# Kernel tuning notes

Hardware: AMD Instinct MI355X
Metric: run time of the kernel (lower is better)

## Reference

```python
import jax, jax.numpy as jnp
import numpy as np

B, M, N = 4, 1024, 4096
DQ, DC, H, DH = 512, 512, 8, 64
D = H * DH
NEG = -10000000.0


def setup_inputs() -> dict:
    key = jax.random.key(0)
    ks = jax.random.split(key, 7)
    left = jax.random.normal(ks[0], (B, M, DQ), dtype=jnp.float32)
    right = jax.random.normal(ks[1], (B, N, DC), dtype=jnp.float32)
    mask = jax.random.randint(ks[2], (B, M, N), 0, 2).astype(bool)
    # learned params (torch Linear stores weight as (out,in); we store (in,out))
    Wq = jax.random.normal(ks[3], (DQ, D), dtype=jnp.float32) * (DQ ** -0.5)
    Wkv = jax.random.normal(ks[4], (DC, 2 * D), dtype=jnp.float32) * (DC ** -0.5)
    Wout = jax.random.normal(ks[5], (D, DQ), dtype=jnp.float32) * (D ** -0.5)
    bout = jax.random.normal(ks[6], (DQ,), dtype=jnp.float32) * 0.01
    return {"left": left, "right": right, "mask": mask,
            "Wq": Wq, "Wkv": Wkv, "Wout": Wout, "bout": bout}


def reference(left, right, mask, Wq, Wkv, Wout, bout):
    scale = DH ** -0.5
    q = left @ Wq                      # (B, M, D)
    kv = right @ Wkv                   # (B, N, 2D)
    k, v = jnp.split(kv, 2, axis=-1)   # (B, N, D) each
    q = q.reshape(B, M, H, DH).transpose(0, 2, 1, 3)  # (B, H, M, DH)
    k = k.reshape(B, N, H, DH).transpose(0, 2, 1, 3)  # (B, H, N, DH)
    v = v.reshape(B, N, H, DH).transpose(0, 2, 1, 3)  # (B, H, N, DH)
    sim = scale * jnp.einsum('bhmd,bhnd->bhmn', q, k)  # (B, H, M, N)
    sim = jnp.where(mask[:, None, :, :], sim, NEG)
    attn = jax.nn.softmax(sim, axis=-1)
    out = jnp.einsum('bhmn,bhnd->bhmd', attn, v)       # (B, H, M, DH)
    out = out.transpose(0, 2, 1, 3).reshape(B, M, D)
    return out @ Wout + bout           # (B, M, DQ)
```

## Files before the change

kernel.cpp:

```cpp
#include <hip/hip_runtime.h>

typedef _Float16 f16;
typedef __attribute__((ext_vector_type(8))) _Float16 half8;
typedef __attribute__((ext_vector_type(4))) _Float16 half4;
typedef __attribute__((ext_vector_type(4))) float floatx4;
typedef unsigned int uint32;
typedef __attribute__((ext_vector_type(4))) uint32 uint4v;

#define MFMA16(a, b, c) __builtin_amdgcn_mfma_f32_16x16x32_f16((a), (b), (c), 0, 0, 0)

constexpr int B_ = 4, M_ = 1024, N_ = 4096, DQ_ = 512, DC_ = 512, H_ = 8, DH_ = 64, D_ = 512;
constexpr int KP_ = 576;
constexpr int VP_ = 4224;
constexpr int NSPLIT = 4;
constexpr float QSC_ = 0.18033688011112042f;

typedef __attribute__((address_space(1))) const void glds_g;
typedef __attribute__((address_space(3))) void glds_l;
__device__ __forceinline__ void g2lds16(const void* g, void* l) {
    __builtin_amdgcn_global_load_lds((glds_g*)g, (glds_l*)l, 16, 0, 0);
}

__device__ __forceinline__ void wtr_tile(const float* __restrict__ src, f16* __restrict__ dst,
                                         int Nout, int bx, int by, int tid) {
    __shared__ __align__(16) f16 Ts[64][72];
    const int n0 = bx * 64, k0 = by * 64;
    {
        int kr = tid >> 2, q4 = tid & 3;
        const float* sp = src + (size_t)(k0 + kr) * Nout + n0 + q4 * 16;
        float4 x0 = *(const float4*)(sp + 0), x1 = *(const float4*)(sp + 4);
        float4 x2 = *(const float4*)(sp + 8), x3 = *(const float4*)(sp + 12);
        half8 h0, h1;
        h0[0]=(f16)x0.x; h0[1]=(f16)x0.y; h0[2]=(f16)x0.z; h0[3]=(f16)x0.w;
        h0[4]=(f16)x1.x; h0[5]=(f16)x1.y; h0[6]=(f16)x1.z; h0[7]=(f16)x1.w;
        h1[0]=(f16)x2.x; h1[1]=(f16)x2.y; h1[2]=(f16)x2.z; h1[3]=(f16)x2.w;
        h1[4]=(f16)x3.x; h1[5]=(f16)x3.y; h1[6]=(f16)x3.z; h1[7]=(f16)x3.w;
        *(half8*)&Ts[kr][q4 * 16] = h0;
        *(half8*)&Ts[kr][q4 * 16 + 8] = h1;
    }
    __syncthreads();
    {
        int nr = tid >> 2, q = tid & 3;
        half8 h0, h1;
#pragma unroll
        for (int j = 0; j < 8; j++) { h0[j] = Ts[q * 16 + j][nr]; h1[j] = Ts[q * 16 + 8 + j][nr]; }
        f16* dp = dst + (size_t)(n0 + nr) * 512 + k0 + q * 16;
        *(half8*)(dp + 0) = h0;
        *(half8*)(dp + 8) = h1;
    }
}

__global__ __launch_bounds__(256)
void prep_k(const void* __restrict__ mask, uint32* __restrict__ bits,
            const float* __restrict__ Wq, f16* __restrict__ wqt,
            const float* __restrict__ Wkv, f16* __restrict__ wkvt,
            const float* __restrict__ Wout, f16* __restrict__ woutt) {
    const int blk = blockIdx.x, tid = threadIdx.x;
    if (blk < 4096) {
        __shared__ int s_bad;
        if (tid == 0) s_bad = 0;
        __syncthreads();
        const uint32* w = (const uint32*)mask + (size_t)blk * 1024;
        int bad = 0;
#pragma unroll
        for (int j = 0; j < 4; j++) bad |= (w[tid * 4 + j] & 0xFFFFFFFEu) != 0u;
        if (bad) s_bad = 1;
        __syncthreads();
        const bool bytes_mode = s_bad != 0;
        uint32 v = 0;
        if (bytes_mode) {
            uint4 x = *(const uint4*)((const unsigned char*)mask + (size_t)blk * 4096 + tid * 16);
            uint32 ws_[4] = {x.x, x.y, x.z, x.w};
#pragma unroll
            for (int k = 0; k < 4; k++)
#pragma unroll
                for (int bb = 0; bb < 4; bb++)
                    v |= (((ws_[k] >> (8 * bb)) & 0xFFu) != 0u ? 1u : 0u) << (k * 4 + bb);
        } else {
            const uint4* p = (const uint4*)((const uint32*)mask + (size_t)blk * 4096 + tid * 16);
            uint4 x0 = p[0], x1 = p[1], x2 = p[2], x3 = p[3];
            uint32 ws_[16] = {x0.x, x0.y, x0.z, x0.w, x1.x, x1.y, x1.z, x1.w,
                              x2.x, x2.y, x2.z, x2.w, x3.x, x3.y, x3.z, x3.w};
#pragma unroll
            for (int k = 0; k < 16; k++) v |= (ws_[k] != 0u ? 1u : 0u) << k;
        }
        uint32 other = (uint32)__shfl_xor((int)v, 1);
        if ((tid & 1) == 0)
            bits[(size_t)blk * 128 + (tid >> 1)] = v | (other << 16);
    } else if (blk < 4160) {
        int r = blk - 4096;
        wtr_tile(Wq, wqt, 512, r & 7, r >> 3, tid);
    } else if (blk < 4288) {
        int r = blk - 4160;
        wtr_tile(Wkv, wkvt, 1024, r & 15, r >> 4, tid);
    } else {
        int r = blk - 4288;
        wtr_tile(Wout, woutt, 512, r & 7, r >> 3, tid);
    }
}

__global__ __launch_bounds__(256)
void gemmqkv_k(const float* __restrict__ left, const f16* __restrict__ wqt,
               const float* __restrict__ right, const f16* __restrict__ wkvt,
               f16* __restrict__ qb, f16* __restrict__ kb, f16* __restrict__ vt) {
    __shared__ __align__(16) f16 As[128 * 64];
    __shared__ __align__(16) f16 Bs[128 * 64];
    const int hw = blockIdx.x, tid = threadIdx.x;
    const int lane = tid & 63, wave = tid >> 6;
    const int qd = lane >> 4, l16 = lane & 15;
    const int wm = wave >> 1, wn = wave & 1;

    int mode;
    const float* F32b; const f16* F16b; size_t m0, n0;
    bool f32A;
    if (hw < 1024) {
        const int xcd = hw & 7, s = hw >> 3;
        const int mi_ = (s >> 6) * 64 + xcd * 8 + (s & 7);
        const int ni_ = (s >> 3) & 7;
        size_t rows = (size_t)mi_ * 128, cols = (size_t)ni_ * 128;
        F32b = right + rows * 512;
        F16b = wkvt + cols * 512;
        if (cols < 512) { mode = 0; f32A = true;  m0 = rows; n0 = cols; }
        else            { mode = 1; f32A = false; m0 = cols; n0 = rows; }
    } else {
        const int r = hw - 1024;
        const int xcd = r & 7, s = r >> 3;
        const int mi_ = xcd * 4 + (s & 3);
        const int ni_ = s >> 2;
        mode = 2; f32A = true;
        m0 = (size_t)mi_ * 128; n0 = (size_t)ni_ * 128;
        F32b = left + m0 * 512;
        F16b = wqt + n0 * 512;
    }
    f16* LF32 = f32A ? As : Bs;
    f16* LF16 = f32A ? Bs : As;

    int crow[4], ccol8[4];
    size_t g16off[4];
    f16* g16dst[4];
#pragma unroll
    for (int i = 0; i < 4; i++) {
        int c = i * 256 + wave * 64 + lane;
        int row = c >> 3, col8 = (c & 7) ^ (row & 7);
        crow[i] = row; ccol8[i] = col8;
        g16off[i] = (size_t)row * 512 + col8 * 8;
        g16dst[i] = LF16 + (size_t)(i * 256 + wave * 64) * 8;
    }

    floatx4 acc[4][4] = {};
    float4 ra[4][2];

#pragma unroll
    for (int i = 0; i < 4; i++) {
        const float* sp = F32b + (size_t)crow[i] * 512 + ccol8[i] * 8;
        ra[i][0] = *(const float4*)sp;
        ra[i][1] = *(const float4*)(sp + 4);
    }

    for (int k0 = 0; k0 < 512; k0 += 64) {
        __syncthreads();
#pragma unroll
        for (int i = 0; i < 4; i++) g2lds16(F16b + g16off[i] + k0, g16dst[i]);
#pragma unroll
        for (int i = 0; i < 4; i++) {
            half8 hh;
            hh[0] = (f16)ra[i][0].x; hh[1] = (f16)ra[i][0].y;
            hh[2] = (f16)ra[i][0].z; hh[3] = (f16)ra[i][0].w;
            hh[4] = (f16)ra[i][1].x; hh[5] = (f16)ra[i][1].y;
            hh[6] = (f16)ra[i][1].z; hh[7] = (f16)ra[i][1].w;
            *(half8*)&LF32[(size_t)(i * 256 + wave * 64 + lane) * 8] = hh;
        }
        __syncthreads();
        if (k0 + 64 < 512) {
#pragma unroll
            for (int i = 0; i < 4; i++) {
                const float* sp = F32b + (size_t)crow[i] * 512 + (k0 + 64) + ccol8[i] * 8;
                ra[i][0] = *(const float4*)sp;
                ra[i][1] = *(const float4*)(sp + 4);
            }
        }
#pragma unroll
        for (int kk = 0; kk < 2; kk++) {
            half8 a[4], b[4];
#pragma unroll
            for (int t = 0; t < 4; t++) {
                int rowa = wm * 64 + t * 16 + l16;
                int rowb = wn * 64 + t * 16 + l16;
                int pa8 = ((kk * 4 + qd) ^ (rowa & 7)) * 8;
                int pb8 = ((kk * 4 + qd) ^ (rowb & 7)) * 8;
                a[t] = *(const half8*)&As[rowa * 64 + pa8];
                b[t] = *(const half8*)&Bs[rowb * 64 + pb8];
            }
#pragma unroll
            for (int mt = 0; mt < 4; mt++)
#pragma unroll
                for (int nt = 0; nt < 4; nt++)
                    acc[mt][nt] = MFMA16(a[mt], b[nt], acc[mt][nt]);
        }
    }

#pragma unroll
    for (int mt = 0; mt < 4; mt++)
#pragma unroll
        for (int nt = 0; nt < 4; nt++)
#pragma unroll
            for (int r = 0; r < 4; r++) {
                size_t mi = m0 + wm * 64 + mt * 16 + qd * 4 + r;
                size_t ni = n0 + wn * 64 + nt * 16 + l16;
                float v = acc[mt][nt][r];
                if (mode == 2) {
                    qb[mi * 512 + ni] = (f16)v;
                } else if (mode == 0) {
                    kb[mi * KP_ + ni] = (f16)v;
                } else {
                    int dcol = (int)mi - 512;
                    int hh = dcol >> 6, dh = dcol & 63;
                    size_t bb = ni >> 12, nn = ni & 4095;
                    vt[((bb * H_ + hh) * (size_t)DH_ + dh) * VP_ + nn] = (f16)v;
                }
            }
}

__global__ __launch_bounds__(512, 8)
void attn_k(const f16* __restrict__ Qb, const f16* __restrict__ Kb,
            const f16* __restrict__ Vt, const uint32* __restrict__ mb,
            float* __restrict__ Op, float* __restrict__ Lp) {
    const int tid = threadIdx.x;
    const int lane = tid & 63, wave = tid >> 6;
    const int qd = lane >> 4, l16 = lane & 15;
    const int bh = blockIdx.x, b = bh >> 3, h = bh & 7;
    const int z = blockIdx.z;
    constexpr int iters = N_ / (64 * NSPLIT);
    const int n_base = z * iters * 64;
    const int m_base = blockIdx.y * 128 + wave * 16;

    __shared__ __align__(16) f16 Ks[2][64 * 64];
    __shared__ __align__(16) f16 Vs[2][64 * 64];

    half8 q0, q1;
    {
        const f16* qrow = Qb + ((size_t)(b * M_ + m_base + l16)) * D_ + h * DH_;
        half8 r0 = *(const half8*)(qrow + qd * 8);
        half8 r1 = *(const half8*)(qrow + 32 + qd * 8);
#pragma unroll
        for (int j = 0; j < 8; j++) {
            q0[j] = (f16)((float)r0[j] * QSC_);
            q1[j] = (f16)((float)r1[j] * QSC_);
        }
    }

    floatx4 ot[4] = {};
    float l_acc = 0.0f;

    const uint32* mrow = mb + ((size_t)(b * M_ + m_base + l16)) * (N_ / 32);

    const int srow = wave * 8;
    const int r8 = lane >> 3, p8 = lane & 7;
    const int gc8 = p8 ^ r8;
    const f16* kg = Kb + ((size_t)(b * N_) + srow + r8) * KP_ + h * DH_ + gc8 * 8;
    const f16* vg = Vt + ((size_t)(bh * DH_) + srow + r8) * VP_ + gc8 * 8;

    auto stage = [&](int buf, int n0) {
        g2lds16(kg + (size_t)n0 * KP_, &Ks[buf][srow * 64]);
        g2lds16(vg + n0, &Vs[buf][srow * 64]);
    };

    stage(0, n_base);
    uint2 mmc = *(const uint2*)(mrow + (n_base >> 5));
    int cur = 0;

    const int swz = (l16 & 7);

    for (int it = 0; it < iters; it++) {
        const int n0 = n_base + it * 64;
        __syncthreads();
        uint2 mmn;
        if (it + 1 < iters) {
            stage(cur ^ 1, n0 + 64);
            mmn = *(const uint2*)(mrow + ((n0 + 64) >> 5));
        }

        const uint32 u0 = mmc.x >> (qd * 4);
        const uint32 u1 = mmc.y >> (qd * 4);

        uint32 pk[4][2];
#pragma unroll
        for (int s = 0; s < 4; s++) {
            const int ro = (s * 16 + l16) * 64;
            half8 k0 = *(const half8*)&Ks[cur][ro + ((qd ^ swz) * 8)];
            half8 k1 = *(const half8*)&Ks[cur][ro + (((4 + qd) ^ swz) * 8)];
            floatx4 t = {};
            t = MFMA16(k0, q0, t);
            t = MFMA16(k1, q1, t);
            uint32 us = (s & 2 ? u1 : u0) >> ((s & 1) * 16);
            float e0 = __builtin_amdgcn_exp2f(t[0]);
            float e1 = __builtin_amdgcn_exp2f(t[1]);
            float e2 = __builtin_amdgcn_exp2f(t[2]);
            float e3 = __builtin_amdgcn_exp2f(t[3]);
            e0 = (us & 1u) ? e0 : 0.0f;
            e1 = (us & 2u) ? e1 : 0.0f;
            e2 = (us & 4u) ? e2 : 0.0f;
            e3 = (us & 8u) ? e3 : 0.0f;
            l_acc += (e0 + e1) + (e2 + e3);
            pk[s][0] = __builtin_bit_cast(uint32, __builtin_amdgcn_cvt_pkrtz(e0, e1));
            pk[s][1] = __builtin_bit_cast(uint32, __builtin_amdgcn_cvt_pkrtz(e2, e3));
        }

        half8 pa[2];
#pragma unroll
        for (int hh = 0; hh < 2; hh++) {
            uint32 w0, w1, w2, w3;
            {
                auto a = __builtin_amdgcn_permlane32_swap(pk[2 * hh][0], pk[2 * hh + 1][0], false, false);
                auto c = __builtin_amdgcn_permlane16_swap(a[0], a[1], false, false);
                w0 = c[0]; w2 = c[1];
            }
            {
                auto a = __builtin_amdgcn_permlane32_swap(pk[2 * hh][1], pk[2 * hh + 1][1], false, false);
                auto c = __builtin_amdgcn_permlane16_swap(a[0], a[1], false, false);
                w1 = c[0]; w3 = c[1];
            }
            uint4v wv = {w0, w1, w2, w3};
            pa[hh] = __builtin_bit_cast(half8, wv);
        }

#pragma unroll
        for (int sd = 0; sd < 4; sd++) {
            const int ro = (sd * 16 + l16) * 64;
            half8 v0 = *(const half8*)&Vs[cur][ro + ((qd ^ swz) * 8)];
            half8 v1 = *(const half8*)&Vs[cur][ro + (((4 + qd) ^ swz) * 8)];
            ot[sd] = MFMA16(v0, pa[0], ot[sd]);
            ot[sd] = MFMA16(v1, pa[1], ot[sd]);
        }
        mmc = mmn;
        cur ^= 1;
    }

    l_acc += __shfl_xor(l_acc, 16);
    l_acc += __shfl_xor(l_acc, 32);

    {
        size_t row = (size_t)(z * 32 + bh) * M_ + m_base + l16;
        float* op = Op + row * DH_ + qd * 4;
#pragma unroll
        for (int sd = 0; sd < 4; sd++)
            __builtin_nontemporal_store(ot[sd], (floatx4*)(op + sd * 16));
        if (qd == 0) __builtin_nontemporal_store(l_acc, Lp + row);
    }
}

__global__ __launch_bounds__(256)
void comb_k(const float* __restrict__ Op, const float* __restrict__ Lp, f16* __restrict__ Ob,
            int nsp) {
    int i = blockIdx.x * 256 + threadIdx.x;
    int d4 = i & 15, m = (i >> 4) & 1023, bh = i >> 14;
    float nx = 0.f, ny = 0.f, nz = 0.f, nw = 0.f, den = 0.f;
    for (int s = 0; s < nsp; s++) {
        size_t row = ((size_t)s * 32 + bh) * M_ + m;
        float4 x = *(const float4*)(Op + row * DH_ + d4 * 4);
        nx += x.x; ny += x.y; nz += x.z; nw += x.w;
        den += Lp[row];
    }
    float r = 1.0f / den;
    int b = bh >> 3, h = bh & 7;
    f16* o = Ob + ((size_t)(b * M_ + m)) * D_ + h * DH_ + d4 * 4;
    half4 hv; hv[0] = (f16)(nx * r); hv[1] = (f16)(ny * r); hv[2] = (f16)(nz * r); hv[3] = (f16)(nw * r);
    *(half4*)o = hv;
}

__global__ __launch_bounds__(256)
void gemmout_k(const f16* __restrict__ A, const f16* __restrict__ Bt,
               float* __restrict__ Fout, const float* __restrict__ bias) {
    __shared__ __align__(16) f16 As[2][64 * 64];
    __shared__ __align__(16) f16 Bs[2][64 * 64];
    const int tid = threadIdx.x;
    const int lane = tid & 63, wave = tid >> 6;
    const int qd = lane >> 4, l16 = lane & 15;
    const int wm = wave >> 1, wn = wave & 1;
    const size_t m0 = (size_t)blockIdx.x * 64;
    const size_t n0 = (size_t)blockIdx.y * 64;

    size_t goff[2];
    f16 *la[2][2], *lb[2][2];
#pragma unroll
    for (int i = 0; i < 2; i++) {
        int c = i * 256 + wave * 64 + lane;
        int row = c >> 3, col8 = (c & 7) ^ (row & 7);
        goff[i] = (size_t)row * 512 + col8 * 8;
        la[0][i] = &As[0][(size_t)(i * 256 + wave * 64) * 8];
        la[1][i] = &As[1][(size_t)(i * 256 + wave * 64) * 8];
        lb[0][i] = &Bs[0][(size_t)(i * 256 + wave * 64) * 8];
        lb[1][i] = &Bs[1][(size_t)(i * 256 + wave * 64) * 8];
    }
    const f16* Ab = A + m0 * 512;
    const f16* Bb = Bt + n0 * 512;

    floatx4 acc[2][2] = {};

#pragma unroll
    for (int i = 0; i < 2; i++) g2lds16(Ab + goff[i], la[0][i]);
#pragma unroll
    for (int i = 0; i < 2; i++) g2lds16(Bb + goff[i], lb[0][i]);
    int cur = 0;

    for (int k0 = 0; k0 < 512; k0 += 64) {
        __syncthreads();
        if (k0 + 64 < 512) {
            const int nxt = cur ^ 1;
#pragma unroll
            for (int i = 0; i < 2; i++) g2lds16(Ab + goff[i] + k0 + 64, la[nxt][i]);
#pragma unroll
            for (int i = 0; i < 2; i++) g2lds16(Bb + goff[i] + k0 + 64, lb[nxt][i]);
        }
        const f16* Ac = &As[cur][0];
        const f16* Bc = &Bs[cur][0];
#pragma unroll
        for (int kk = 0; kk < 2; kk++) {
            half8 a[2], b[2];
#pragma unroll
            for (int t = 0; t < 2; t++) {
                int rowa = wm * 32 + t * 16 + l16;
                int rowb = wn * 32 + t * 16 + l16;
                int pa8 = ((kk * 4 + qd) ^ (rowa & 7)) * 8;
                int pb8 = ((kk * 4 + qd) ^ (rowb & 7)) * 8;
                a[t] = *(const half8*)&Ac[rowa * 64 + pa8];
                b[t] = *(const half8*)&Bc[rowb * 64 + pb8];
            }
#pragma unroll
            for (int mt = 0; mt < 2; mt++)
#pragma unroll
                for (int nt = 0; nt < 2; nt++)
                    acc[mt][nt] = MFMA16(a[mt], b[nt], acc[mt][nt]);
        }
        cur ^= 1;
    }

#pragma unroll
    for (int mt = 0; mt < 2; mt++)
#pragma unroll
        for (int nt = 0; nt < 2; nt++)
#pragma unroll
            for (int r = 0; r < 4; r++) {
                size_t row = m0 + wm * 32 + mt * 16 + qd * 4 + r;
                size_t col = n0 + wn * 32 + nt * 16 + l16;
                Fout[row * 512 + col] = acc[mt][nt][r] + bias[col];
            }
}

extern "C" void kernel_launch(void* const* d_in, const int* in_sizes, int n_in,
                              void* d_out, int out_size, void* d_ws, size_t ws_size,
                              hipStream_t stream) {
    const float* left  = (const float*)d_in[0];
    const float* right = (const float*)d_in[1];
    const void*  mask  = d_in[2];
    const float* Wq    = (const float*)d_in[3];
    const float* Wkv   = (const float*)d_in[4];
    const float* Wout  = (const float*)d_in[5];
    const float* bout  = (const float*)d_in[6];

    char* ws = (char*)d_ws;
    size_t off = 0;
    auto take = [&](size_t bytes) { char* p = ws + off; off += (bytes + 255) & ~(size_t)255; return p; };
    uint32* mbits = (uint32*)take((size_t)B_ * M_ * N_ / 8);
    f16* woutt = (f16*)take((size_t)D_ * DQ_ * 2);
    f16* qb    = (f16*)take((size_t)B_ * M_ * D_ * 2);
    f16* kb    = (f16*)take((size_t)B_ * N_ * KP_ * 2);
    f16* vt    = (f16*)take((size_t)B_ * H_ * DH_ * VP_ * 2);
    f16* ob    = (f16*)take((size_t)B_ * M_ * D_ * 2);
    char* pool = (char*)take((size_t)34 * 1024 * 1024);
    f16* wqt    = (f16*)pool;
    f16* wkvt   = (f16*)(pool + (size_t)1 * 1024 * 1024);
    float* Op   = (float*)pool;
    float* Lp   = (float*)(pool + (size_t)NSPLIT * 32 * M_ * DH_ * 4);

    prep_k<<<4352, 256, 0, stream>>>(mask, mbits, Wq, wqt, Wkv, wkvt, Wout, woutt);
    gemmqkv_k<<<1152, 256, 0, stream>>>(left, wqt, right, wkvt, qb, kb, vt);
    attn_k<<<dim3(32, 8, NSPLIT), 512, 0, stream>>>(qb, kb, vt, mbits, Op, Lp);
    comb_k<<<2048, 256, 0, stream>>>(Op, Lp, ob, NSPLIT);
    gemmout_k<<<dim3(64, 8), 256, 0, stream>>>(ob, woutt, (float*)d_out, bout);
}
```

Before: 266.5 us.

## Enlarge QKV GEMM tiles to 256x128 with 512-thread blocks

The Q/KV projection GEMM moves from 128x128 tiles with 256 threads to 256-row activation tiles by 128-column weight tiles with 512 threads. This halves the grid and doubles reuse of each weight panel per block. The register prefetch of the fp32 activations for the next k-step is dropped; loads now happen inside the loop just before the LDS store. That removes some register pressure but exposes global load latency before each barrier.

```diff
diff --git a/kernel.cpp b/kernel.cpp
--- a/kernel.cpp
+++ b/kernel.cpp
@@ -99,126 +99,120 @@
     }
 }
 
-__global__ __launch_bounds__(256)
+__global__ __launch_bounds__(512, 4)
 void gemmqkv_k(const float* __restrict__ left, const f16* __restrict__ wqt,
                const float* __restrict__ right, const f16* __restrict__ wkvt,
                f16* __restrict__ qb, f16* __restrict__ kb, f16* __restrict__ vt) {
-    __shared__ __align__(16) f16 As[128 * 64];
-    __shared__ __align__(16) f16 Bs[128 * 64];
+    __shared__ __align__(16) f16 Rs[256 * 64];
+    __shared__ __align__(16) f16 Ws[128 * 64];
     const int hw = blockIdx.x, tid = threadIdx.x;
     const int lane = tid & 63, wave = tid >> 6;
     const int qd = lane >> 4, l16 = lane & 15;
-    const int wm = wave >> 1, wn = wave & 1;
-
-    int mode;
-    const float* F32b; const f16* F16b; size_t m0, n0;
-    bool f32A;
-    if (hw < 1024) {
+    const int wr = wave >> 1;
+    const int ww = wave & 1;
+
+    int mode; size_t rbase, wbase;
+    const float* Rg; const f16* Wg;
+    if (hw < 512) {
         const int xcd = hw & 7, s = hw >> 3;
-        const int mi_ = (s >> 6) * 64 + xcd * 8 + (s & 7);
-        const int ni_ = (s >> 3) & 7;
-        size_t rows = (size_t)mi_ * 128, cols = (size_t)ni_ * 128;
-        F32b = right + rows * 512;
-        F16b = wkvt + cols * 512;
-        if (cols < 512) { mode = 0; f32A = true;  m0 = rows; n0 = cols; }
-        else            { mode = 1; f32A = false; m0 = cols; n0 = rows; }
+        const int wpan = s & 7, rpan = xcd * 8 + (s >> 3);
+        rbase = (size_t)rpan * 256; wbase = (size_t)wpan * 128;
+        Rg = right; Wg = wkvt;
+        mode = (wpan < 4) ? 0 : 1;
     } else {
-        const int r = hw - 1024;
+        const int r = hw - 512;
         const int xcd = r & 7, s = r >> 3;
-        const int mi_ = xcd * 4 + (s & 3);
-        const int ni_ = s >> 2;
-        mode = 2; f32A = true;
-        m0 = (size_t)mi_ * 128; n0 = (size_t)ni_ * 128;
-        F32b = left + m0 * 512;
-        F16b = wqt + n0 * 512;
-    }
-    f16* LF32 = f32A ? As : Bs;
-    f16* LF16 = f32A ? Bs : As;
-
-    int crow[4], ccol8[4];
-    size_t g16off[4];
-    f16* g16dst[4];
+        const int wpan = s & 3, rpan = xcd * 2 + (s >> 2);
+        rbase = (size_t)rpan * 256; wbase = (size_t)wpan * 128;
+        Rg = left; Wg = wqt;
+        mode = 2;
+    }
+    const float* Rb = Rg + rbase * 512;
+    const f16*  Wb = Wg + wbase * 512;
+
+    size_t wgoff[2]; f16* wdst[2];
+#pragma unroll
+    for (int i = 0; i < 2; i++) {
+        int c = i * 512 + tid;
+        int row = c >> 3, col8 = (c & 7) ^ (row & 7);
+        wgoff[i] = (size_t)row * 512 + col8 * 8;
+        wdst[i] = Ws + (size_t)(i * 512 + wave * 64) * 8;
+    }
+    int rrow[4], rcol8[4];
 #pragma unroll
     for (int i = 0; i < 4; i++) {
-        int c = i * 256 + wave * 64 + lane;
-        int row = c >> 3, col8 = (c & 7) ^ (row & 7);
-        crow[i] = row; ccol8[i] = col8;
-        g16off[i] = (size_t)row * 512 + col8 * 8;
-        g16dst[i] = LF16 + (size_t)(i * 256 + wave * 64) * 8;
+        int c = i * 512 + tid;
+        rrow[i] = c >> 3; rcol8[i] = (c & 7) ^ (rrow[i] & 7);
     }
 
     floatx4 acc[4][4] = {};
-    float4 ra[4][2];
-
-#pragma unroll
-    for (int i = 0; i < 4; i++) {
-        const float* sp = F32b + (size_t)crow[i] * 512 + ccol8[i] * 8;
-        ra[i][0] = *(const float4*)sp;
-        ra[i][1] = *(const float4*)(sp + 4);
-    }
 
     for (int k0 = 0; k0 < 512; k0 += 64) {
         __syncthreads();
 #pragma unroll
-        for (int i = 0; i < 4; i++) g2lds16(F16b + g16off[i] + k0, g16dst[i]);
+        for (int i = 0; i < 2; i++) g2lds16(Wb + wgoff[i] + k0, wdst[i]);
 #pragma unroll
         for (int i = 0; i < 4; i++) {
+            const float* sp = Rb + (size_t)rrow[i] * 512 + k0 + rcol8[i] * 8;
+            float4 x0 = *(const float4*)sp, x1 = *(const float4*)(sp + 4);
             half8 hh;
-            hh[0] = (f16)ra[i][0].x; hh[1] = (f16)ra[i][0].y;
-            hh[2] = (f16)ra[i][0].z; hh[3] = (f16)ra[i][0].w;
-            hh[4] = (f16)ra[i][1].x; hh[5] = (f16)ra[i][1].y;
-            hh[6] = (f16)ra[i][1].z; hh[7] = (f16)ra[i][1].w;
-            *(half8*)&LF32[(size_t)(i * 256 + wave * 64 + lane) * 8] = hh;
-        }
-        __syncthreads();
-        if (k0 + 64 < 512) {
-#pragma unroll
-            for (int i = 0; i < 4; i++) {
-                const float* sp = F32b + (size_t)crow[i] * 512 + (k0 + 64) + ccol8[i] * 8;
-                ra[i][0] = *(const float4*)sp;
-                ra[i][1] = *(const float4*)(sp + 4);
-            }
-        }
+            hh[0]=(f16)x0.x; hh[1]=(f16)x0.y; hh[2]=(f16)x0.z; hh[3]=(f16)x0.w;
+            hh[4]=(f16)x1.x; hh[5]=(f16)x1.y; hh[6]=(f16)x1.z; hh[7]=(f16)x1.w;
+            *(half8*)&Rs[(size_t)(i * 512 + tid) * 8] = hh;
+        }
+        __syncthreads();
 #pragma unroll
         for (int kk = 0; kk < 2; kk++) {
-            half8 a[4], b[4];
+            half8 rf[4], wf[4];
 #pragma unroll
             for (int t = 0; t < 4; t++) {
-                int rowa = wm * 64 + t * 16 + l16;
-                int rowb = wn * 64 + t * 16 + l16;
-                int pa8 = ((kk * 4 + qd) ^ (rowa & 7)) * 8;
-                int pb8 = ((kk * 4 + qd) ^ (rowb & 7)) * 8;
-                a[t] = *(const half8*)&As[rowa * 64 + pa8];
-                b[t] = *(const half8*)&Bs[rowb * 64 + pb8];
-            }
-#pragma unroll
-            for (int mt = 0; mt < 4; mt++)
-#pragma unroll
-                for (int nt = 0; nt < 4; nt++)
-                    acc[mt][nt] = MFMA16(a[mt], b[nt], acc[mt][nt]);
-        }
-    }
-
-#pragma unroll
-    for (int mt = 0; mt < 4; mt++)
-#pragma unroll
-        for (int nt = 0; nt < 4; nt++)
-#pragma unroll
-            for (int r = 0; r < 4; r++) {
-                size_t mi = m0 + wm * 64 + mt * 16 + qd * 4 + r;
-                size_t ni = n0 + wn * 64 + nt * 16 + l16;
-                float v = acc[mt][nt][r];
-                if (mode == 2) {
-                    qb[mi * 512 + ni] = (f16)v;
-                } else if (mode == 0) {
-                    kb[mi * KP_ + ni] = (f16)v;
-                } else {
-                    int dcol = (int)mi - 512;
-                    int hh = dcol >> 6, dh = dcol & 63;
+                int rowr = wr * 64 + t * 16 + l16;
+                int roww = ww * 64 + t * 16 + l16;
+                rf[t] = *(const half8*)&Rs[rowr * 64 + (((kk * 4 + qd) ^ (rowr & 7)) * 8)];
+                wf[t] = *(const half8*)&Ws[roww * 64 + (((kk * 4 + qd) ^ (roww & 7)) * 8)];
+            }
+            if (mode == 1) {
+#pragma unroll
+                for (int mt = 0; mt < 4; mt++)
+#pragma unroll
+                    for (int nt = 0; nt < 4; nt++)
+                        acc[mt][nt] = MFMA16(wf[mt], rf[nt], acc[mt][nt]);
+            } else {
+#pragma unroll
+                for (int mt = 0; mt < 4; mt++)
+#pragma unroll
+                    for (int nt = 0; nt < 4; nt++)
+                        acc[mt][nt] = MFMA16(rf[mt], wf[nt], acc[mt][nt]);
+            }
+        }
+    }
+
+    if (mode == 1) {
+#pragma unroll
+        for (int mt = 0; mt < 4; mt++)
+#pragma unroll
+            for (int nt = 0; nt < 4; nt++)
+#pragma unroll
+                for (int r = 0; r < 4; r++) {
+                    int dcol = (int)wbase + ww * 64 + mt * 16 + qd * 4 + r - 512;
+                    size_t ni = rbase + wr * 64 + nt * 16 + l16;
+                    int hh2 = dcol >> 6, dh = dcol & 63;
                     size_t bb = ni >> 12, nn = ni & 4095;
-                    vt[((bb * H_ + hh) * (size_t)DH_ + dh) * VP_ + nn] = (f16)v;
+                    vt[((bb * H_ + hh2) * (size_t)DH_ + dh) * VP_ + nn] = (f16)acc[mt][nt][r];
                 }
-            }
+    } else {
+#pragma unroll
+        for (int mt = 0; mt < 4; mt++)
+#pragma unroll
+            for (int nt = 0; nt < 4; nt++)
+#pragma unroll
+                for (int r = 0; r < 4; r++) {
+                    size_t mi = rbase + wr * 64 + mt * 16 + qd * 4 + r;
+                    size_t ni = wbase + ww * 64 + nt * 16 + l16;
+                    if (mode == 2) qb[mi * 512 + ni] = (f16)acc[mt][nt][r];
+                    else           kb[mi * KP_ + ni] = (f16)acc[mt][nt][r];
+                }
+    }
 }
 
 __global__ __launch_bounds__(512, 8)
@@ -474,7 +468,7 @@
     float* Lp   = (float*)(pool + (size_t)NSPLIT * 32 * M_ * DH_ * 4);
 
     prep_k<<<4352, 256, 0, stream>>>(mask, mbits, Wq, wqt, Wkv, wkvt, Wout, woutt);
-    gemmqkv_k<<<1152, 256, 0, stream>>>(left, wqt, right, wkvt, qb, kb, vt);
+    gemmqkv_k<<<576, 512, 0, stream>>>(left, wqt, right, wkvt, qb, kb, vt);
     attn_k<<<dim3(32, 8, NSPLIT), 512, 0, stream>>>(qb, kb, vt, mbits, Op, Lp);
     comb_k<<<2048, 256, 0, stream>>>(Op, Lp, ob, NSPLIT);
     gemmout_k<<<dim3(64, 8), 256, 0, stream>>>(ob, woutt, (float*)d_out, bout);
```

New measurement: 474.4 us. +78.0%, slower.
